# Optimization experiments

Hardware: AMD Instinct MI355X
Metric: run time of the kernel (lower is better)

The kernel has to match this reference:

```python
import jax, jax.numpy as jnp
import numpy as np
from jax import lax

K = 3  # kernel_size


def _leaky(x):
    return jnp.where(x >= 0, x, 0.1 * x)


def _conv3x3(x, w, b):
    # x: (B,C,H,W), w: (O,C,3,3)
    out = lax.conv_general_dilated(x, w, (1, 1), [(1, 1), (1, 1)],
                                   dimension_numbers=('NCHW', 'OIHW', 'NCHW'))
    return out + b[None, :, None, None]


def _da_conv(x, d, kw1, kw2, cw, cb, ca1, ca2):
    # per-sample dynamic depthwise conv + 1x1 conv + channel attention
    b, c, h, w = x.shape
    p = (K - 1) // 2
    # predicted per-(sample,channel) KxK kernels: (b, c*K*K) -> (b*c, 1, K, K)
    kern = (_leaky(d @ kw1.T) @ kw2.T).reshape(b * c, 1, K, K)
    out = lax.conv_general_dilated(x.reshape(1, b * c, h, w), kern, (1, 1),
                                   [(p, p), (p, p)], feature_group_count=b * c,
                                   dimension_numbers=('NCHW', 'OIHW', 'NCHW'))
    out = _leaky(out).reshape(b, c, h, w)
    # 1x1 conv with bias
    out = jnp.einsum('bchw,oc->bohw', out, cw) + cb[None, :, None, None]
    # CA layer: sigmoid(W2 @ leaky(W1 @ d)) per sample
    att = jax.nn.sigmoid(_leaky(d @ ca1.T) @ ca2.T)  # (b, c_out)
    return out + x * att[:, :, None, None]


def _forward(x, d,
             da1_kw1, da1_kw2, da1_cw, da1_cb, da1_ca1, da1_ca2,
             da2_kw1, da2_kw2, da2_cw, da2_cb, da2_ca1, da2_ca2,
             conv1_w, conv1_b, conv2_w, conv2_b, conv3_w, conv3_b,
             add_w1, add_w2):
    out = _leaky(_da_conv(x, d, da1_kw1, da1_kw2, da1_cw, da1_cb, da1_ca1, da1_ca2))
    out = _leaky(_conv3x3(out, conv1_w, conv1_b))
    # additive map: (b, 1024) -> (b,1,32,32) -> nearest-upsample to (H,W)
    add = (_leaky(d @ add_w1.T) @ add_w2.T).reshape(-1, 1, 32, 32)
    H = out.shape[-1]
    idx = jnp.arange(H) * 32 // H  # PyTorch 'nearest' index rule
    add = add[:, :, idx[:, None], idx[None, :]]
    out = out + add
    out = _conv3x3(out, conv2_w, conv2_b)
    out = _leaky(_da_conv(out, d, da2_kw1, da2_kw2, da2_cw, da2_cb, da2_ca1, da2_ca2))
    return _conv3x3(out, conv3_w, conv3_b) + x


def setup_inputs() -> dict:
    B, C, H, W = 8, 64, 192, 192
    RED = 8
    key = jax.random.key(0)
    ks = jax.random.split(key, 24)
    n = lambda k, shape, s=0.05: jax.random.normal(k, shape, jnp.float32) * s
    inp = {
        'x': jax.random.normal(ks[0], (B, C, H, W), jnp.float32),
        'd': jax.random.normal(ks[1], (B, C), jnp.float32),
    }
    for i, pfx in enumerate(['da1', 'da2']):
        base = 2 + i * 6
        inp[f'{pfx}_kw1'] = n(ks[base + 0], (64, 64))
        inp[f'{pfx}_kw2'] = n(ks[base + 1], (C * K * K, 64))
        inp[f'{pfx}_cw'] = n(ks[base + 2], (C, C))   # 1x1 conv weight (O,I)
        inp[f'{pfx}_cb'] = n(ks[base + 3], (C,))
        inp[f'{pfx}_ca1'] = n(ks[base + 4], (C // RED, 64))
        inp[f'{pfx}_ca2'] = n(ks[base + 5], (C, C // RED))
    for i, pfx in enumerate(['conv1', 'conv2', 'conv3']):
        inp[f'{pfx}_w'] = n(ks[14 + 2 * i], (C, C, K, K))
        inp[f'{pfx}_b'] = n(ks[15 + 2 * i], (C,))
    inp['add_w1'] = n(ks[20], (64, 64))
    inp['add_w2'] = n(ks[21], (32 * 32, 64))
    return inp


def reference(x, d,
              da1_kw1, da1_kw2, da1_cw, da1_cb, da1_ca1, da1_ca2,
              da2_kw1, da2_kw2, da2_cw, da2_cb, da2_ca1, da2_ca2,
              conv1_w, conv1_b, conv2_w, conv2_b, conv3_w, conv3_b,
              add_w1, add_w2):
    return _forward(x, d,
                    da1_kw1, da1_kw2, da1_cw, da1_cb, da1_ca1, da1_ca2,
                    da2_kw1, da2_kw2, da2_cw, da2_cb, da2_ca1, da2_ca2,
                    conv1_w, conv1_b, conv2_w, conv2_b, conv3_w, conv3_b,
                    add_w1, add_w2)
```

## Files before the change

### kernel.cpp

```cpp
#include <hip/hip_runtime.h>
#include <math.h>

#define B_ 8
#define C_ 64
#define H_ 192
#define W_ 192
#define HW_ (H_*W_)

typedef __attribute__((ext_vector_type(8))) short bf16x8;
typedef __attribute__((ext_vector_type(4))) float f32x4;
typedef __attribute__((ext_vector_type(4))) unsigned short u16x4;
typedef __attribute__((ext_vector_type(8))) unsigned short u16x8;
typedef __attribute__((ext_vector_type(4))) unsigned int u32x4;

__device__ __forceinline__ float lk(float v){ return v >= 0.f ? v : 0.1f*v; }
__device__ __forceinline__ float bf2f(unsigned short h){ return __uint_as_float(((unsigned)h)<<16); }
__device__ __forceinline__ unsigned short f2bf(float f){
    unsigned u = __float_as_uint(f);
    return (unsigned short)((u + 0x7fffu + ((u>>16)&1u)) >> 16);
}
__device__ __forceinline__ f32x4 mfma16(bf16x8 a, bf16x8 b, f32x4 c){
    return __builtin_amdgcn_mfma_f32_16x16x32_bf16(a, b, c, 0, 0, 0);
}

__device__ __forceinline__ void xcd_decomp(int L, int& b, int& h0, int& w0){
    b = L & 7;
    int t = L >> 3;
    h0 = (t / 12) * 16;
    w0 = (t % 12) * 16;
}

__global__ __launch_bounds__(256) void k_small(
    const float* __restrict__ d,
    const float* __restrict__ kw1a, const float* __restrict__ kw2a,
    const float* __restrict__ ca1a, const float* __restrict__ ca2a,
    const float* __restrict__ kw1b, const float* __restrict__ kw2b,
    const float* __restrict__ ca1b, const float* __restrict__ ca2b,
    const float* __restrict__ aw1,  const float* __restrict__ aw2,
    float* __restrict__ kern1, float* __restrict__ att1,
    float* __restrict__ kern2, float* __restrict__ att2,
    float* __restrict__ addm)
{
    int b = blockIdx.x, tid = threadIdx.x;
    __shared__ float sd[64], sv[64], su[8];
    if (tid < 64) sd[tid] = d[b*64 + tid];
    __syncthreads();
    if (tid < 64){ float s=0.f; for(int k=0;k<64;k++) s += sd[k]*kw1a[tid*64+k]; sv[tid]=lk(s); }
    if (tid >= 64 && tid < 72){ int r=tid-64; float s=0.f; for(int k=0;k<64;k++) s += sd[k]*ca1a[r*64+k]; su[r]=lk(s); }
    __syncthreads();
    for (int i=tid;i<576;i+=256){ float s=0.f; for(int j=0;j<64;j++) s += sv[j]*kw2a[i*64+j]; kern1[b*576+i]=s; }
    if (tid < 64){ float s=0.f; for(int r=0;r<8;r++) s += su[r]*ca2a[tid*8+r]; att1[b*64+tid]=1.f/(1.f+expf(-s)); }
    __syncthreads();
    if (tid < 64){ float s=0.f; for(int k=0;k<64;k++) s += sd[k]*kw1b[tid*64+k]; sv[tid]=lk(s); }
    if (tid >= 64 && tid < 72){ int r=tid-64; float s=0.f; for(int k=0;k<64;k++) s += sd[k]*ca1b[r*64+k]; su[r]=lk(s); }
    __syncthreads();
    for (int i=tid;i<576;i+=256){ float s=0.f; for(int j=0;j<64;j++) s += sv[j]*kw2b[i*64+j]; kern2[b*576+i]=s; }
    if (tid < 64){ float s=0.f; for(int r=0;r<8;r++) s += su[r]*ca2b[tid*8+r]; att2[b*64+tid]=1.f/(1.f+expf(-s)); }
    __syncthreads();
    if (tid < 64){ float s=0.f; for(int k=0;k<64;k++) s += sd[k]*aw1[tid*64+k]; sv[tid]=lk(s); }
    __syncthreads();
    for (int i=tid;i<1024;i+=256){ float s=0.f; for(int j=0;j<64;j++) s += sv[j]*aw2[i*64+j]; addm[b*1024+i]=s; }
}

__global__ __launch_bounds__(256) void k_prep(
    const float* __restrict__ w1, const float* __restrict__ w2, const float* __restrict__ w3,
    const float* __restrict__ cw1, const float* __restrict__ cw2,
    unsigned short* __restrict__ wA1, unsigned short* __restrict__ wA2, unsigned short* __restrict__ wA3,
    unsigned short* __restrict__ cwA1, unsigned short* __restrict__ cwA2)
{
    int blk = blockIdx.x;
    if (blk < 192){
        const float* w = (blk < 64) ? w1 : (blk < 128) ? w2 : w3;
        unsigned short* wA = (blk < 64) ? wA1 : (blk < 128) ? wA2 : wA3;
        int oc = blk & 63;
        for (int i = threadIdx.x; i < 576; i += 256){
            int t = i >> 6, ic = i & 63;
            wA[oc*576 + i] = f2bf(w[oc*576 + ic*9 + t]);
        }
    } else {
        int i = (blk - 192)*256 + threadIdx.x;
        if (i < 4096) cwA1[i] = f2bf(cw1[i]);
        else          cwA2[i-4096] = f2bf(cw2[i-4096]);
    }
}

__global__ __launch_bounds__(256) void k_xprep(const float* __restrict__ xf, unsigned short* __restrict__ xb){
    int L = blockIdx.x;
    int b = L & 7, px0 = (L >> 3)*256;
    int tid = threadIdx.x;
    __shared__ unsigned short ts[256*64];
    int q = tid >> 5, p = tid & 31;
    #pragma unroll 1
    for (int j=0; j<8; j++){
        int px = p + 32*j;
        u16x8 o;
        #pragma unroll
        for (int i=0; i<8; i++)
            o[i] = f2bf(xf[((size_t)(b*64 + q*8 + i))*HW_ + px0 + px]);
        *(u16x8*)&ts[px*64 + ((q ^ (px&7))*8)] = o;
    }
    __syncthreads();
    int k = tid & 7, pg = tid >> 3;
    #pragma unroll 1
    for (int j=0; j<8; j++){
        int px = pg + 32*j;
        u32x4 v = *(const u32x4*)&ts[px*64 + ((k ^ (px&7))*8)];
        *(u32x4*)&xb[((size_t)(b*HW_) + px0 + px)*64 + k*8] = v;
    }
}

__device__ __forceinline__ void stage64(const unsigned short* __restrict__ in,
                                        unsigned short* xs, int b, int h0, int w0, int tid)
{
    for (int gi = tid; gi < 18*18*8; gi += 256){
        int pix = gi >> 3, j = gi & 7;
        int r = pix/18, col = pix - r*18;
        int gh = h0 - 1 + r, gw = w0 - 1 + col;
        u32x4 v = {0u,0u,0u,0u};
        if (gh >= 0 && gh < H_ && gw >= 0 && gw < W_)
            v = *(const u32x4*)&in[((size_t)(b*HW_ + gh*W_ + gw))*64 + j*8];
        *(u32x4*)&xs[pix*64 + ((j ^ (pix&7))*8)] = v;
    }
}

__device__ __forceinline__ void conv_main(const unsigned short* xs,
                                          const unsigned short* __restrict__ wbase,
                                          bf16x8 afr[2][2],
                                          int n, int g, int rowbase, f32x4 acc[2][8])
{
    #pragma unroll 1
    for (int t=0; t<9; t++){
        bf16x8 nxt[2][2];
        if (t < 8){
            #pragma unroll
            for (int mf=0; mf<2; mf++)
                #pragma unroll
                for (int kf=0; kf<2; kf++)
                    nxt[mf][kf] = *(const bf16x8*)(wbase + mf*(16*576) + (t+1)*64 + kf*32);
        }
        int dy = t/3, dx = t - dy*3;
        #pragma unroll
        for (int r=0; r<8; r++){
            int pix = (rowbase + r + dy)*18 + (n + dx);
            int sw = pix & 7;
            #pragma unroll
            for (int kf=0; kf<2; kf++){
                bf16x8 bfr = *(const bf16x8*)&xs[pix*64 + (((kf*4+g) ^ sw)*8)];
                acc[0][r] = mfma16(afr[0][kf], bfr, acc[0][r]);
                acc[1][r] = mfma16(afr[1][kf], bfr, acc[1][r]);
            }
        }
        if (t < 8){
            #pragma unroll
            for (int mf=0; mf<2; mf++)
                #pragma unroll
                for (int kf=0; kf<2; kf++) afr[mf][kf] = nxt[mf][kf];
        }
    }
}

template<int MODE>
__global__ __launch_bounds__(256) void k_conv(
    const unsigned short* __restrict__ in,
    const unsigned short* __restrict__ wA,
    const float* __restrict__ bias,
    const float* __restrict__ addm,
    unsigned short* __restrict__ outb)
{
    int b, h0, w0; xcd_decomp(blockIdx.x, b, h0, w0);
    int tid = threadIdx.x;
    __shared__ unsigned short xs[18*18*64];

    int lane = tid & 63, wv = tid >> 6;
    int n = lane & 15, g = lane >> 4;
    int ochalf = (wv & 1)*32, rowbase = (wv >> 1)*8;

    stage64(in, xs, b, h0, w0, tid);

    const unsigned short* wbase = wA + (size_t)(ochalf + n)*576 + g*8;
    bf16x8 afr[2][2];
    #pragma unroll
    for (int mf=0; mf<2; mf++)
        #pragma unroll
        for (int kf=0; kf<2; kf++)
            afr[mf][kf] = *(const bf16x8*)(wbase + mf*(16*576) + kf*32);

    __syncthreads();

    f32x4 acc[2][8];
    f32x4 zz = {0.f,0.f,0.f,0.f};
    #pragma unroll
    for (int mf=0; mf<2; mf++)
        #pragma unroll
        for (int r=0; r<8; r++) acc[mf][r] = zz;

    conv_main(xs, wbase, afr, n, g, rowbase, acc);

    #pragma unroll
    for (int r=0; r<8; r++){
        int h = h0 + rowbase + r, w = w0 + n;
        float addv = 0.f;
        if (MODE == 0) addv = addm[b*1024 + (h/6)*32 + (w/6)];
        #pragma unroll
        for (int mf=0; mf<2; mf++){
            int oc0 = ochalf + mf*16 + g*4;
            f32x4 v = acc[mf][r];
            f32x4 b4 = *(const f32x4*)&bias[oc0];
            u16x4 o;
            #pragma unroll
            for (int j=0;j<4;j++){
                float val = v[j] + b4[j];
                if (MODE == 0) val = lk(val) + addv;
                o[j] = f2bf(val);
            }
            *(u16x4*)&outb[((size_t)(b*HW_ + h*W_ + w))*64 + oc0] = o;
        }
    }
}

__global__ __launch_bounds__(256) void kc3(
    const unsigned short* __restrict__ in,
    const unsigned short* __restrict__ wA,
    const float* __restrict__ bias,
    const float* __restrict__ xres,
    float* __restrict__ outf)
{
    int b, h0, w0; xcd_decomp(blockIdx.x, b, h0, w0);
    int tid = threadIdx.x;
    __shared__ unsigned short xs[18*18*64];

    int lane = tid & 63, wv = tid >> 6;
    int n = lane & 15, g = lane >> 4;
    int ochalf = (wv & 1)*32, rowbase = (wv >> 1)*8;

    stage64(in, xs, b, h0, w0, tid);

    const unsigned short* wbase = wA + (size_t)(ochalf + n)*576 + g*8;
    bf16x8 afr[2][2];
    #pragma unroll
    for (int mf=0; mf<2; mf++)
        #pragma unroll
        for (int kf=0; kf<2; kf++)
            afr[mf][kf] = *(const bf16x8*)(wbase + mf*(16*576) + kf*32);

    __syncthreads();

    f32x4 acc[2][8];
    f32x4 zz = {0.f,0.f,0.f,0.f};
    #pragma unroll
    for (int mf=0; mf<2; mf++)
        #pragma unroll
        for (int r=0; r<8; r++) acc[mf][r] = zz;

    conv_main(xs, wbase, afr, n, g, rowbase, acc);

    __syncthreads();
    unsigned short* ys = xs;

    #pragma unroll
    for (int mf=0; mf<2; mf++){
        int oc0 = ochalf + mf*16 + g*4;
        int sw = ((oc0 >> 2) & 3) << 2;
        f32x4 b4 = *(const f32x4*)&bias[oc0];
        #pragma unroll
        for (int r=0; r<8; r++){
            int px = (rowbase + r)*16 + n;
            f32x4 v = acc[mf][r];
            #pragma unroll
            for (int j=0; j<4; j++)
                ys[(oc0 + j)*256 + (px ^ sw)] = f2bf(v[j] + b4[j]);
        }
    }
    __syncthreads();

    int q = lane & 3, rr = lane >> 2;
    #pragma unroll 1
    for (int pass=0; pass<16; pass++){
        int oc = wv + pass*4;
        int sw = ((oc >> 2) & 3) << 2;
        int px = (rr*16 + q*4) ^ sw;
        u16x4 t = *(const u16x4*)&ys[oc*256 + px];
        size_t gidx = ((size_t)(b*C_ + oc))*HW_ + (size_t)(h0 + rr)*W_ + w0 + q*4;
        f32x4 xv = *(const f32x4*)&xres[gidx];
        f32x4 o;
        #pragma unroll
        for (int j=0; j<4; j++) o[j] = bf2f(t[j]) + xv[j];
        *(f32x4*)&outf[gidx] = o;
    }
}

__device__ __forceinline__ void dw_pass(const unsigned short* xs, const float* skT,
                                        int r0, int cc, int gg, bf16x8 pbv[4])
{
    float acc[4][8];
    #pragma unroll
    for (int k=0;k<4;k++)
        #pragma unroll
        for (int i=0;i<8;i++) acc[k][i] = 0.f;

    #pragma unroll
    for (int ir=0; ir<6; ir++){
        float f[3][8];
        #pragma unroll
        for (int dx=0; dx<3; dx++){
            int spix = (r0+ir)*18 + cc + dx;
            bf16x8 v = *(const bf16x8*)&xs[spix*64 + ((gg ^ (spix&7))*8)];
            #pragma unroll
            for (int i=0;i<8;i++) f[dx][i] = bf2f((unsigned short)v[i]);
        }
        #pragma unroll
        for (int k=0;k<4;k++){
            if (ir >= k && ir <= k+2){
                int dy = ir - k;
                #pragma unroll
                for (int dx=0; dx<3; dx++){
                    f32x4 ka = *(const f32x4*)&skT[(dy*3+dx)*64 + gg*8];
                    f32x4 kb = *(const f32x4*)&skT[(dy*3+dx)*64 + gg*8 + 4];
                    #pragma unroll
                    for (int i=0;i<4;i++){
                        acc[k][i]   = fmaf(f[dx][i],   ka[i], acc[k][i]);
                        acc[k][i+4] = fmaf(f[dx][i+4], kb[i], acc[k][i+4]);
                    }
                }
            }
        }
    }
    #pragma unroll
    for (int k=0;k<4;k++){
        bf16x8 pb;
        #pragma unroll
        for (int i=0;i<8;i++) pb[i] = (short)f2bf(lk(acc[k][i]));
        pbv[k] = pb;
    }
}

__global__ __launch_bounds__(256) void k_da(
    const unsigned short* __restrict__ xb,
    const float* __restrict__ kern,
    const float* __restrict__ att,
    const unsigned short* __restrict__ cwA,
    const float* __restrict__ cb,
    unsigned short* __restrict__ outb)
{
    int b, h0, w0; xcd_decomp(blockIdx.x, b, h0, w0);
    int tid = threadIdx.x;
    __shared__ unsigned short xs[18*18*64];
    __shared__ float skernT[576];

    int lane = tid & 63, wv = tid >> 6;
    int cc = lane & 15, g = lane >> 4;
    int r0 = wv*4;

    for (int i = tid; i < 576; i += 256)
        skernT[i] = kern[b*576 + (i & 63)*9 + (i >> 6)];

    stage64(xb, xs, b, h0, w0, tid);

    bf16x8 afr[4][2];
    #pragma unroll
    for (int mf=0; mf<4; mf++)
        #pragma unroll
        for (int kf=0; kf<2; kf++)
            afr[mf][kf] = *(const bf16x8*)&cwA[(size_t)(mf*16 + cc)*64 + kf*32 + g*8];

    __syncthreads();

    f32x4 accm[4][4];
    f32x4 zz = {0.f,0.f,0.f,0.f};
    #pragma unroll
    for (int k=0;k<4;k++)
        #pragma unroll
        for (int mf=0; mf<4; mf++) accm[k][mf] = zz;

    bf16x8 pbv[4];
    dw_pass(xs, skernT, r0, cc, g, pbv);
    #pragma unroll
    for (int k=0;k<4;k++)
        #pragma unroll
        for (int mf=0; mf<4; mf++)
            accm[k][mf] = mfma16(afr[mf][0], pbv[k], accm[k][mf]);

    dw_pass(xs, skernT, r0, cc, 4+g, pbv);
    #pragma unroll
    for (int k=0;k<4;k++)
        #pragma unroll
        for (int mf=0; mf<4; mf++)
            accm[k][mf] = mfma16(afr[mf][1], pbv[k], accm[k][mf]);

    #pragma unroll
    for (int k=0;k<4;k++){
        int r = r0 + k;
        int h = h0 + r, w = w0 + cc;
        int spix = (r+1)*18 + (cc+1);
        int sw7 = spix & 7;
        #pragma unroll
        for (int mf=0; mf<4; mf++){
            int oc0 = mf*16 + g*4;
            f32x4 v = accm[k][mf];
            f32x4 cb4 = *(const f32x4*)&cb[oc0];
            f32x4 at4 = *(const f32x4*)&att[b*64 + oc0];
            int jg = (oc0 >> 3) ^ sw7;
            u16x4 xr = *(const u16x4*)&xs[spix*64 + jg*8 + (oc0 & 7)];
            u16x4 o;
            #pragma unroll
            for (int j=0; j<4; j++){
                float val = v[j] + cb4[j] + bf2f(xr[j])*at4[j];
                o[j] = f2bf(lk(val));
            }
            *(u16x4*)&outb[((size_t)(b*HW_ + h*W_ + w))*64 + oc0] = o;
        }
    }
}

extern "C" void kernel_launch(void* const* d_in, const int* in_sizes, int n_in,
                              void* d_out, int out_size, void* d_ws, size_t ws_size,
                              hipStream_t stream)
{
    const float* x       = (const float*)d_in[0];
    const float* d       = (const float*)d_in[1];
    const float* da1_kw1 = (const float*)d_in[2];
    const float* da1_kw2 = (const float*)d_in[3];
    const float* da1_cw  = (const float*)d_in[4];
    const float* da1_cb  = (const float*)d_in[5];
    const float* da1_ca1 = (const float*)d_in[6];
    const float* da1_ca2 = (const float*)d_in[7];
    const float* da2_kw1 = (const float*)d_in[8];
    const float* da2_kw2 = (const float*)d_in[9];
    const float* da2_cw  = (const float*)d_in[10];
    const float* da2_cb  = (const float*)d_in[11];
    const float* da2_ca1 = (const float*)d_in[12];
    const float* da2_ca2 = (const float*)d_in[13];
    const float* conv1_w = (const float*)d_in[14];
    const float* conv1_b = (const float*)d_in[15];
    const float* conv2_w = (const float*)d_in[16];
    const float* conv2_b = (const float*)d_in[17];
    const float* conv3_w = (const float*)d_in[18];
    const float* conv3_b = (const float*)d_in[19];
    const float* add_w1  = (const float*)d_in[20];
    const float* add_w2  = (const float*)d_in[21];

    float* wsf   = (float*)d_ws;
    float* kern1 = wsf;
    float* att1  = wsf + 4608;
    float* kern2 = wsf + 5120;
    float* att2  = wsf + 9728;
    float* addm  = wsf + 10240;
    unsigned short* wsb  = (unsigned short*)(wsf + 18432);
    unsigned short* wA1  = wsb;
    unsigned short* wA2  = wA1 + 36864;
    unsigned short* wA3  = wA2 + 36864;
    unsigned short* cwA1 = wA3 + 36864;
    unsigned short* cwA2 = cwA1 + 4096;
    unsigned short* xbuf = cwA2 + 4096;
    const size_t N = (size_t)B_*HW_*64;
    unsigned short* buf0 = xbuf + N;
    unsigned short* buf1 = buf0 + N;

    k_small<<<B_, 256, 0, stream>>>(d, da1_kw1, da1_kw2, da1_ca1, da1_ca2,
                                    da2_kw1, da2_kw2, da2_ca1, da2_ca2,
                                    add_w1, add_w2, kern1, att1, kern2, att2, addm);
    k_prep<<<224, 256, 0, stream>>>(conv1_w, conv2_w, conv3_w, da1_cw, da2_cw,
                                    wA1, wA2, wA3, cwA1, cwA2);
    k_xprep<<<1152, 256, 0, stream>>>(x, xbuf);

    k_da<<<1152, 256, 0, stream>>>(xbuf, kern1, att1, cwA1, da1_cb, buf0);
    k_conv<0><<<1152, 256, 0, stream>>>(buf0, wA1, conv1_b, addm, buf1);
    k_conv<1><<<1152, 256, 0, stream>>>(buf1, wA2, conv2_b, nullptr, xbuf);
    k_da<<<1152, 256, 0, stream>>>(xbuf, kern2, att2, cwA2, da2_cb, buf0);
    kc3<<<1152, 256, 0, stream>>>(buf0, wA3, conv3_b, x, (float*)d_out);

    (void)in_sizes; (void)n_in; (void)out_size; (void)ws_size;
}
```

Baseline: 298.1 us.

## Make 3x3 conv kernels persistent with register-resident weights and prefetched tiles

Replaces the 1152-block 3x3 conv launches with 256 persistent blocks, each looping over 4-5 spatial tiles of one batch image. All nine taps of the weight fragments are loaded into registers once per block, and the next tile's halo is prefetched into registers while the current tile is computed, so global loads overlap the MFMA work. The cost is much higher register pressure (launch_bounds 256,1), only 256 blocks on a 256-CU part with an uneven 5/4 tile split, and the loss of the XCD-aware block mapping.

Measured after the change: 300.4 us. No clear change (+0.8%).

```diff
diff --git a/kernel.cpp b/kernel.cpp
--- a/kernel.cpp
+++ b/kernel.cpp
@@ -109,65 +109,42 @@
     }
 }
 
-__device__ __forceinline__ void stage64(const unsigned short* __restrict__ in,
-                                        unsigned short* xs, int b, int h0, int w0, int tid)
-{
-    for (int gi = tid; gi < 18*18*8; gi += 256){
-        int pix = gi >> 3, j = gi & 7;
+__device__ __forceinline__ void stage_load(const unsigned short* __restrict__ in,
+                                           u32x4 st[11], int b, int h0, int w0, int tid)
+{
+    #pragma unroll
+    for (int i=0; i<11; i++){
+        int e = tid + i*256; if (e > 2591) e = 2591;
+        int pix = e >> 3, j = e & 7;
         int r = pix/18, col = pix - r*18;
         int gh = h0 - 1 + r, gw = w0 - 1 + col;
         u32x4 v = {0u,0u,0u,0u};
         if (gh >= 0 && gh < H_ && gw >= 0 && gw < W_)
             v = *(const u32x4*)&in[((size_t)(b*HW_ + gh*W_ + gw))*64 + j*8];
-        *(u32x4*)&xs[pix*64 + ((j ^ (pix&7))*8)] = v;
-    }
-}
-
-__device__ __forceinline__ void conv_main(const unsigned short* xs,
-                                          const unsigned short* __restrict__ wbase,
-                                          bf16x8 afr[2][2],
-                                          int n, int g, int rowbase, f32x4 acc[2][8])
-{
-    #pragma unroll 1
-    for (int t=0; t<9; t++){
-        bf16x8 nxt[2][2];
-        if (t < 8){
-            #pragma unroll
-            for (int mf=0; mf<2; mf++)
-                #pragma unroll
-                for (int kf=0; kf<2; kf++)
-                    nxt[mf][kf] = *(const bf16x8*)(wbase + mf*(16*576) + (t+1)*64 + kf*32);
-        }
-        int dy = t/3, dx = t - dy*3;
-        #pragma unroll
-        for (int r=0; r<8; r++){
-            int pix = (rowbase + r + dy)*18 + (n + dx);
-            int sw = pix & 7;
-            #pragma unroll
-            for (int kf=0; kf<2; kf++){
-                bf16x8 bfr = *(const bf16x8*)&xs[pix*64 + (((kf*4+g) ^ sw)*8)];
-                acc[0][r] = mfma16(afr[0][kf], bfr, acc[0][r]);
-                acc[1][r] = mfma16(afr[1][kf], bfr, acc[1][r]);
-            }
-        }
-        if (t < 8){
-            #pragma unroll
-            for (int mf=0; mf<2; mf++)
-                #pragma unroll
-                for (int kf=0; kf<2; kf++) afr[mf][kf] = nxt[mf][kf];
-        }
+        st[i] = v;
+    }
+}
+__device__ __forceinline__ void stage_write(const u32x4 st[11], unsigned short* xs, int tid)
+{
+    #pragma unroll
+    for (int i=0; i<11; i++){
+        int e = tid + i*256; if (e > 2591) e = 2591;
+        int pix = e >> 3, j = e & 7;
+        *(u32x4*)&xs[pix*64 + ((j ^ (pix&7))*8)] = st[i];
     }
 }
 
 template<int MODE>
-__global__ __launch_bounds__(256) void k_conv(
+__global__ __launch_bounds__(256, 1) void k_convP(
     const unsigned short* __restrict__ in,
     const unsigned short* __restrict__ wA,
     const float* __restrict__ bias,
     const float* __restrict__ addm,
     unsigned short* __restrict__ outb)
 {
-    int b, h0, w0; xcd_decomp(blockIdx.x, b, h0, w0);
+    int L = blockIdx.x;
+    int b = L & 7, idx = L >> 3;
+    int nt = (idx < 16) ? 5 : 4;
     int tid = threadIdx.x;
     __shared__ unsigned short xs[18*18*64];
 
@@ -175,57 +152,91 @@
     int n = lane & 15, g = lane >> 4;
     int ochalf = (wv & 1)*32, rowbase = (wv >> 1)*8;
 
-    stage64(in, xs, b, h0, w0, tid);
-
     const unsigned short* wbase = wA + (size_t)(ochalf + n)*576 + g*8;
-    bf16x8 afr[2][2];
-    #pragma unroll
-    for (int mf=0; mf<2; mf++)
-        #pragma unroll
-        for (int kf=0; kf<2; kf++)
-            afr[mf][kf] = *(const bf16x8*)(wbase + mf*(16*576) + kf*32);
-
-    __syncthreads();
-
-    f32x4 acc[2][8];
-    f32x4 zz = {0.f,0.f,0.f,0.f};
-    #pragma unroll
-    for (int mf=0; mf<2; mf++)
-        #pragma unroll
-        for (int r=0; r<8; r++) acc[mf][r] = zz;
-
-    conv_main(xs, wbase, afr, n, g, rowbase, acc);
-
-    #pragma unroll
-    for (int r=0; r<8; r++){
-        int h = h0 + rowbase + r, w = w0 + n;
-        float addv = 0.f;
-        if (MODE == 0) addv = addm[b*1024 + (h/6)*32 + (w/6)];
-        #pragma unroll
-        for (int mf=0; mf<2; mf++){
-            int oc0 = ochalf + mf*16 + g*4;
-            f32x4 v = acc[mf][r];
-            f32x4 b4 = *(const f32x4*)&bias[oc0];
-            u16x4 o;
-            #pragma unroll
-            for (int j=0;j<4;j++){
-                float val = v[j] + b4[j];
-                if (MODE == 0) val = lk(val) + addv;
-                o[j] = f2bf(val);
+    bf16x8 wfr[9][2][2];
+    #pragma unroll
+    for (int t=0; t<9; t++)
+        #pragma unroll
+        for (int mf=0; mf<2; mf++)
+            #pragma unroll
+            for (int kf=0; kf<2; kf++)
+                wfr[t][mf][kf] = *(const bf16x8*)(wbase + mf*(16*576) + t*64 + kf*32);
+
+    u32x4 st[11];
+    {
+        int t0 = idx;
+        stage_load(in, st, b, (t0/12)*16, (t0%12)*16, tid);
+    }
+
+    #pragma unroll 1
+    for (int k=0; k<nt; k++){
+        int t = idx + 32*k;
+        int h0 = (t/12)*16, w0 = (t%12)*16;
+
+        if (k) __syncthreads();
+        stage_write(st, xs, tid);
+        if (k+1 < nt){
+            int tn = idx + 32*(k+1);
+            stage_load(in, st, b, (tn/12)*16, (tn%12)*16, tid);
+        }
+        __syncthreads();
+
+        f32x4 acc[2][8];
+        f32x4 zz = {0.f,0.f,0.f,0.f};
+        #pragma unroll
+        for (int mf=0; mf<2; mf++)
+            #pragma unroll
+            for (int r=0; r<8; r++) acc[mf][r] = zz;
+
+        #pragma unroll
+        for (int tt=0; tt<9; tt++){
+            int dy = tt/3, dx = tt - dy*3;
+            #pragma unroll
+            for (int r=0; r<8; r++){
+                int pix = (rowbase + r + dy)*18 + (n + dx);
+                int sw = pix & 7;
+                #pragma unroll
+                for (int kf=0; kf<2; kf++){
+                    bf16x8 bfr = *(const bf16x8*)&xs[pix*64 + (((kf*4+g) ^ sw)*8)];
+                    acc[0][r] = mfma16(wfr[tt][0][kf], bfr, acc[0][r]);
+                    acc[1][r] = mfma16(wfr[tt][1][kf], bfr, acc[1][r]);
+                }
             }
-            *(u16x4*)&outb[((size_t)(b*HW_ + h*W_ + w))*64 + oc0] = o;
-        }
-    }
-}
-
-__global__ __launch_bounds__(256) void kc3(
+        }
+
+        #pragma unroll
+        for (int r=0; r<8; r++){
+            int h = h0 + rowbase + r, w = w0 + n;
+            float addv = 0.f;
+            if (MODE == 0) addv = addm[b*1024 + (h/6)*32 + (w/6)];
+            #pragma unroll
+            for (int mf=0; mf<2; mf++){
+                int oc0 = ochalf + mf*16 + g*4;
+                f32x4 v = acc[mf][r];
+                f32x4 b4 = *(const f32x4*)&bias[oc0];
+                u16x4 o;
+                #pragma unroll
+                for (int j=0;j<4;j++){
+                    float val = v[j] + b4[j];
+                    if (MODE == 0) val = lk(val) + addv;
+                    o[j] = f2bf(val);
+                }
+                *(u16x4*)&outb[((size_t)(b*HW_ + h*W_ + w))*64 + oc0] = o;
+            }
+        }
+    }
+}
+
+__global__ __launch_bounds__(256, 1) void kc3P(
     const unsigned short* __restrict__ in,
     const unsigned short* __restrict__ wA,
     const float* __restrict__ bias,
     const float* __restrict__ xres,
     float* __restrict__ outf)
 {
-    int b, h0, w0; xcd_decomp(blockIdx.x, b, h0, w0);
+    int L = blockIdx.x;
+    int b = L & 7, idx = L >> 3;
+    int nt = (idx < 16) ? 5 : 4;
     int tid = threadIdx.x;
     __shared__ unsigned short xs[18*18*64];
 
@@ -233,59 +244,90 @@
     int n = lane & 15, g = lane >> 4;
     int ochalf = (wv & 1)*32, rowbase = (wv >> 1)*8;
 
-    stage64(in, xs, b, h0, w0, tid);
-
     const unsigned short* wbase = wA + (size_t)(ochalf + n)*576 + g*8;
-    bf16x8 afr[2][2];
-    #pragma unroll
-    for (int mf=0; mf<2; mf++)
-        #pragma unroll
-        for (int kf=0; kf<2; kf++)
-            afr[mf][kf] = *(const bf16x8*)(wbase + mf*(16*576) + kf*32);
-
-    __syncthreads();
-
-    f32x4 acc[2][8];
-    f32x4 zz = {0.f,0.f,0.f,0.f};
-    #pragma unroll
-    for (int mf=0; mf<2; mf++)
-        #pragma unroll
-        for (int r=0; r<8; r++) acc[mf][r] = zz;
-
-    conv_main(xs, wbase, afr, n, g, rowbase, acc);
-
-    __syncthreads();
-    unsigned short* ys = xs;
-
-    #pragma unroll
-    for (int mf=0; mf<2; mf++){
-        int oc0 = ochalf + mf*16 + g*4;
-        int sw = ((oc0 >> 2) & 3) << 2;
-        f32x4 b4 = *(const f32x4*)&bias[oc0];
-        #pragma unroll
-        for (int r=0; r<8; r++){
-            int px = (rowbase + r)*16 + n;
-            f32x4 v = acc[mf][r];
-            #pragma unroll
-            for (int j=0; j<4; j++)
-                ys[(oc0 + j)*256 + (px ^ sw)] = f2bf(v[j] + b4[j]);
-        }
-    }
-    __syncthreads();
-
-    int q = lane & 3, rr = lane >> 2;
+    bf16x8 wfr[9][2][2];
+    #pragma unroll
+    for (int t=0; t<9; t++)
+        #pragma unroll
+        for (int mf=0; mf<2; mf++)
+            #pragma unroll
+            for (int kf=0; kf<2; kf++)
+                wfr[t][mf][kf] = *(const bf16x8*)(wbase + mf*(16*576) + t*64 + kf*32);
+
+    u32x4 st[11];
+    {
+        int t0 = idx;
+        stage_load(in, st, b, (t0/12)*16, (t0%12)*16, tid);
+    }
+
     #pragma unroll 1
-    for (int pass=0; pass<16; pass++){
-        int oc = wv + pass*4;
-        int sw = ((oc >> 2) & 3) << 2;
-        int px = (rr*16 + q*4) ^ sw;
-        u16x4 t = *(const u16x4*)&ys[oc*256 + px];
-        size_t gidx = ((size_t)(b*C_ + oc))*HW_ + (size_t)(h0 + rr)*W_ + w0 + q*4;
-        f32x4 xv = *(const f32x4*)&xres[gidx];
-        f32x4 o;
-        #pragma unroll
-        for (int j=0; j<4; j++) o[j] = bf2f(t[j]) + xv[j];
-        *(f32x4*)&outf[gidx] = o;
+    for (int k=0; k<nt; k++){
+        int t = idx + 32*k;
+        int h0 = (t/12)*16, w0 = (t%12)*16;
+
+        if (k) __syncthreads();
+        stage_write(st, xs, tid);
+        if (k+1 < nt){
+            int tn = idx + 32*(k+1);
+            stage_load(in, st, b, (tn/12)*16, (tn%12)*16, tid);
+        }
+        __syncthreads();
+
+        f32x4 acc[2][8];
+        f32x4 zz = {0.f,0.f,0.f,0.f};
+        #pragma unroll
+        for (int mf=0; mf<2; mf++)
+            #pragma unroll
+            for (int r=0; r<8; r++) acc[mf][r] = zz;
+
+        #pragma unroll
+        for (int tt=0; tt<9; tt++){
+            int dy = tt/3, dx = tt - dy*3;
+            #pragma unroll
+            for (int r=0; r<8; r++){
+                int pix = (rowbase + r + dy)*18 + (n + dx);
+                int sw = pix & 7;
+                #pragma unroll
+                for (int kf=0; kf<2; kf++){
+                    bf16x8 bfr = *(const bf16x8*)&xs[pix*64 + (((kf*4+g) ^ sw)*8)];
+                    acc[0][r] = mfma16(wfr[tt][0][kf], bfr, acc[0][r]);
+                    acc[1][r] = mfma16(wfr[tt][1][kf], bfr, acc[1][r]);
+                }
+            }
+        }
+
+        __syncthreads();
+        unsigned short* ys = xs;
+        #pragma unroll
+        for (int mf=0; mf<2; mf++){
+            int oc0 = ochalf + mf*16 + g*4;
+            int sw = ((oc0 >> 2) & 3) << 2;
+            f32x4 b4 = *(const f32x4*)&bias[oc0];
+            #pragma unroll
+            for (int r=0; r<8; r++){
+                int px = (rowbase + r)*16 + n;
+                f32x4 v = acc[mf][r];
+                #pragma unroll
+                for (int j=0; j<4; j++)
+                    ys[(oc0 + j)*256 + (px ^ sw)] = f2bf(v[j] + b4[j]);
+            }
+        }
+        __syncthreads();
+
+        int q = lane & 3, rr = lane >> 2;
+        #pragma unroll 1
+        for (int pass=0; pass<16; pass++){
+            int oc = wv + pass*4;
+            int sw = ((oc >> 2) & 3) << 2;
+            int px = (rr*16 + q*4) ^ sw;
+            u16x4 tv = *(const u16x4*)&ys[oc*256 + px];
+            size_t gidx = ((size_t)(b*C_ + oc))*HW_ + (size_t)(h0 + rr)*W_ + w0 + q*4;
+            f32x4 xv = *(const f32x4*)&xres[gidx];
+            f32x4 o;
+            #pragma unroll
+            for (int j=0; j<4; j++) o[j] = bf2f(tv[j]) + xv[j];
+            *(f32x4*)&outf[gidx] = o;
+        }
     }
 }
 
@@ -354,7 +396,15 @@
     for (int i = tid; i < 576; i += 256)
         skernT[i] = kern[b*576 + (i & 63)*9 + (i >> 6)];
 
-    stage64(xb, xs, b, h0, w0, tid);
+    for (int gi = tid; gi < 18*18*8; gi += 256){
+        int pix = gi >> 3, j = gi & 7;
+        int r = pix/18, col = pix - r*18;
+        int gh = h0 - 1 + r, gw = w0 - 1 + col;
+        u32x4 v = {0u,0u,0u,0u};
+        if (gh >= 0 && gh < H_ && gw >= 0 && gw < W_)
+            v = *(const u32x4*)&xb[((size_t)(b*HW_ + gh*W_ + gw))*64 + j*8];
+        *(u32x4*)&xs[pix*64 + ((j ^ (pix&7))*8)] = v;
+    }
 
     bf16x8 afr[4][2];
     #pragma unroll
@@ -464,10 +514,10 @@
     k_xprep<<<1152, 256, 0, stream>>>(x, xbuf);
 
     k_da<<<1152, 256, 0, stream>>>(xbuf, kern1, att1, cwA1, da1_cb, buf0);
-    k_conv<0><<<1152, 256, 0, stream>>>(buf0, wA1, conv1_b, addm, buf1);
-    k_conv<1><<<1152, 256, 0, stream>>>(buf1, wA2, conv2_b, nullptr, xbuf);
+    k_convP<0><<<256, 256, 0, stream>>>(buf0, wA1, conv1_b, addm, buf1);
+    k_convP<1><<<256, 256, 0, stream>>>(buf1, wA2, conv2_b, nullptr, xbuf);
     k_da<<<1152, 256, 0, stream>>>(xbuf, kern2, att2, cwA2, da2_cb, buf0);
-    kc3<<<1152, 256, 0, stream>>>(buf0, wA3, conv3_b, x, (float*)d_out);
+    kc3P<<<256, 256, 0, stream>>>(buf0, wA3, conv3_b, x, (float*)d_out);
 
     (void)in_sizes; (void)n_in; (void)out_size; (void)ws_size;
 }
```
